# Performance work log

Measured on AMD Instinct MI355X. Metric: run time of the kernel, lower is better.

Reference implementation:

```python
import jax, jax.numpy as jnp
import numpy as np

B, M, L, D = 4, 128, 512, 768
NEG = -1e30


def setup_inputs() -> dict:
    key = jax.random.key(0)
    k1, k2 = jax.random.split(key)
    h = jax.random.normal(k1, (B, L, D), dtype=jnp.float32)
    mention_masks = jax.random.randint(k2, (B, M, L), 0, 2, dtype=jnp.int32)
    return {"h": h, "mention_masks": mention_masks}


def reference(h, mention_masks):
    # h: [B, L, D]; mention_masks: [B, M, L] (0/1)
    # Faithful to: m = (mask == 0).float() * -1e30; (m + h).max(dim=2)
    m = (mention_masks == 0).astype(h.dtype) * NEG          # [B, M, L]
    # broadcast add then max over token dim L -> [B, M, D]
    mention_reprs = jnp.max(h[:, None, :, :] + m[:, :, :, None], axis=2)
    return mention_reprs
```

## Files before the change

### kernel.cpp

```cpp
#include <hip/hip_runtime.h>

#define BB 4
#define MM 128
#define LL 512
#define DD 768
#define NEGF (-1e30f)

__global__ __launch_bounds__(256, 3) void mention_max_part(
    const float* __restrict__ h, const int* __restrict__ mask,
    float* __restrict__ ws)
{
    const int lane = threadIdx.x & 63;
    const int wave = threadIdx.x >> 6;
    const int dch  = blockIdx.x;
    const int mch  = blockIdx.y >> 1;
    const int lh   = blockIdx.y & 1;
    const int b    = blockIdx.z;

    const int d0 = dch * 128 + lane * 2;
    const int m0 = mch * 8;
    const int l0 = lh * 256 + wave * 64;

    const unsigned NEGB = __float_as_uint(NEGF);

    const int* mp = mask + ((size_t)(b * MM + m0)) * LL + l0 + lane;
    unsigned blo[8], bhi[8];
#pragma unroll
    for (int m = 0; m < 8; ++m) {
        unsigned long long bits = __ballot(mp[m * LL] != 0);
        blo[m] = (unsigned)bits;
        bhi[m] = (unsigned)(bits >> 32);
    }

    float2 acc[8];
#pragma unroll
    for (int m = 0; m < 8; ++m) acc[m] = make_float2(NEGF, NEGF);

#pragma unroll
    for (int s = 0; s < 2; ++s) {
        const float2* hp =
            (const float2*)(h + ((size_t)(b * LL + l0 + s * 32)) * DD + d0);
        float2 hreg[32];
#pragma unroll
        for (int i = 0; i < 32; ++i) hreg[i] = hp[(size_t)i * (DD / 2)];

#pragma unroll
        for (int m = 0; m < 8; ++m) {
            const unsigned w32 = s ? bhi[m] : blo[m];
            float ax = acc[m].x, ay = acc[m].y;
#pragma unroll
            for (int i = 0; i < 32; i += 2) {
                const unsigned r0 = (unsigned)((int)(w32 << (31 - i)) >> 31);
                const unsigned r1 = (unsigned)((int)(w32 << (30 - i)) >> 31);
                const float ad0 = __uint_as_float(~r0 & NEGB);
                const float ad1 = __uint_as_float(~r1 & NEGB);
                ax = fmaxf(ax, fmaxf(hreg[i].x + ad0, hreg[i + 1].x + ad1));
                ay = fmaxf(ay, fmaxf(hreg[i].y + ad0, hreg[i + 1].y + ad1));
            }
            acc[m].x = ax;
            acc[m].y = ay;
        }
    }

    __shared__ float2 red[4][8][64];
#pragma unroll
    for (int m = 0; m < 8; ++m) red[wave][m][lane] = acc[m];
    __syncthreads();

#pragma unroll
    for (int r = 0; r < 2; ++r) {
        const int o  = (int)threadIdx.x + r * 256;
        const int m  = o >> 6;
        const int dp = o & 63;
        float2 v = red[0][m][dp];
#pragma unroll
        for (int w = 1; w < 4; ++w) {
            const float2 u = red[w][m][dp];
            v.x = fmaxf(v.x, u.x);
            v.y = fmaxf(v.y, u.y);
        }
        ((float2*)(ws + ((size_t)lh * BB * MM * DD) +
                   ((size_t)(b * MM + m0 + m)) * DD + dch * 128))[dp] = v;
    }
}

__global__ __launch_bounds__(256) void mention_max_merge(
    const float* __restrict__ ws, float* __restrict__ out)
{
    const int i = (int)(blockIdx.x * blockDim.x + threadIdx.x);
    const float4* p0 = (const float4*)ws;
    const float4* p1 = (const float4*)(ws + (size_t)BB * MM * DD);
    const float4 a = p0[i], b = p1[i];
    float4 v;
    v.x = fmaxf(a.x, b.x);
    v.y = fmaxf(a.y, b.y);
    v.z = fmaxf(a.z, b.z);
    v.w = fmaxf(a.w, b.w);
    ((float4*)out)[i] = v;
}

extern "C" void kernel_launch(void* const* d_in, const int* in_sizes, int n_in,
                              void* d_out, int out_size, void* d_ws, size_t ws_size,
                              hipStream_t stream) {
    const float* h    = (const float*)d_in[0];
    const int*   mask = (const int*)d_in[1];
    float*       out  = (float*)d_out;
    float*       ws   = (float*)d_ws;
    dim3 grid1(DD / 128, (MM / 8) * 2, BB);
    mention_max_part<<<grid1, dim3(256), 0, stream>>>(h, mask, ws);
    const int n4 = BB * MM * DD / 4;
    mention_max_merge<<<n4 / 256, dim3(256), 0, stream>>>(ws, out);
}
```

Baseline: 74.18 us.

## Widen per-thread columns to float4 and split tokens into four partial chunks

New measurement: 72.32 us. 1.03x faster.

```diff
diff --git a/kernel.cpp b/kernel.cpp
--- a/kernel.cpp
+++ b/kernel.cpp
@@ -13,56 +13,55 @@
     const int lane = threadIdx.x & 63;
     const int wave = threadIdx.x >> 6;
     const int dch  = blockIdx.x;
-    const int mch  = blockIdx.y >> 1;
-    const int lh   = blockIdx.y & 1;
+    const int mch  = blockIdx.y >> 2;
+    const int lh   = blockIdx.y & 3;
     const int b    = blockIdx.z;
 
-    const int d0 = dch * 128 + lane * 2;
+    const int d0 = dch * 256 + lane * 4;
     const int m0 = mch * 8;
-    const int l0 = lh * 256 + wave * 64;
+    const int l0 = lh * 128 + wave * 32;
 
-    const unsigned NEGB = __float_as_uint(NEGF);
+    const int lclamp = (l0 + lane < LL) ? (l0 + lane) : (LL - 1);
+    const int* mp = mask + ((size_t)(b * MM + m0)) * LL + lclamp;
 
-    const int* mp = mask + ((size_t)(b * MM + m0)) * LL + l0 + lane;
-    unsigned blo[8], bhi[8];
+    unsigned bits[8];
 #pragma unroll
     for (int m = 0; m < 8; ++m) {
-        unsigned long long bits = __ballot(mp[m * LL] != 0);
-        blo[m] = (unsigned)bits;
-        bhi[m] = (unsigned)(bits >> 32);
+        unsigned long long bl = __ballot(mp[m * LL] != 0);
+        bits[m] = (unsigned)__builtin_amdgcn_readfirstlane((int)(unsigned)bl);
     }
 
-    float2 acc[8];
+    float4 acc[8];
 #pragma unroll
-    for (int m = 0; m < 8; ++m) acc[m] = make_float2(NEGF, NEGF);
+    for (int m = 0; m < 8; ++m) acc[m] = make_float4(NEGF, NEGF, NEGF, NEGF);
 
 #pragma unroll
     for (int s = 0; s < 2; ++s) {
-        const float2* hp =
-            (const float2*)(h + ((size_t)(b * LL + l0 + s * 32)) * DD + d0);
-        float2 hreg[32];
+        const float4* hp =
+            (const float4*)(h + ((size_t)(b * LL + l0 + s * 16)) * DD + d0);
+        float4 hreg[16];
 #pragma unroll
-        for (int i = 0; i < 32; ++i) hreg[i] = hp[(size_t)i * (DD / 2)];
+        for (int i = 0; i < 16; ++i) hreg[i] = hp[(size_t)i * (DD / 4)];
 
 #pragma unroll
         for (int m = 0; m < 8; ++m) {
-            const unsigned w32 = s ? bhi[m] : blo[m];
-            float ax = acc[m].x, ay = acc[m].y;
+            const unsigned w = bits[m];
+            float4 a = acc[m];
 #pragma unroll
-            for (int i = 0; i < 32; i += 2) {
-                const unsigned r0 = (unsigned)((int)(w32 << (31 - i)) >> 31);
-                const unsigned r1 = (unsigned)((int)(w32 << (30 - i)) >> 31);
-                const float ad0 = __uint_as_float(~r0 & NEGB);
-                const float ad1 = __uint_as_float(~r1 & NEGB);
-                ax = fmaxf(ax, fmaxf(hreg[i].x + ad0, hreg[i + 1].x + ad1));
-                ay = fmaxf(ay, fmaxf(hreg[i].y + ad0, hreg[i + 1].y + ad1));
+            for (int i = 0; i < 16; i += 2) {
+                const int k = s * 16 + i;
+                const float ad0 = ((w >> k) & 1u) ? 0.0f : NEGF;
+                const float ad1 = ((w >> (k + 1)) & 1u) ? 0.0f : NEGF;
+                a.x = fmaxf(fmaxf(hreg[i].x + ad0, hreg[i + 1].x + ad1), a.x);
+                a.y = fmaxf(fmaxf(hreg[i].y + ad0, hreg[i + 1].y + ad1), a.y);
+                a.z = fmaxf(fmaxf(hreg[i].z + ad0, hreg[i + 1].z + ad1), a.z);
+                a.w = fmaxf(fmaxf(hreg[i].w + ad0, hreg[i + 1].w + ad1), a.w);
             }
-            acc[m].x = ax;
-            acc[m].y = ay;
+            acc[m] = a;
         }
     }
 
-    __shared__ float2 red[4][8][64];
+    __shared__ float4 red[4][8][64];
 #pragma unroll
     for (int m = 0; m < 8; ++m) red[wave][m][lane] = acc[m];
     __syncthreads();
@@ -72,15 +71,17 @@
         const int o  = (int)threadIdx.x + r * 256;
         const int m  = o >> 6;
         const int dp = o & 63;
-        float2 v = red[0][m][dp];
+        float4 v = red[0][m][dp];
 #pragma unroll
         for (int w = 1; w < 4; ++w) {
-            const float2 u = red[w][m][dp];
+            const float4 u = red[w][m][dp];
             v.x = fmaxf(v.x, u.x);
             v.y = fmaxf(v.y, u.y);
+            v.z = fmaxf(v.z, u.z);
+            v.w = fmaxf(v.w, u.w);
         }
-        ((float2*)(ws + ((size_t)lh * BB * MM * DD) +
-                   ((size_t)(b * MM + m0 + m)) * DD + dch * 128))[dp] = v;
+        ((float4*)(ws + ((size_t)lh * BB * MM * DD) +
+                   ((size_t)(b * MM + m0 + m)) * DD + dch * 256))[dp] = v;
     }
 }
 
@@ -88,14 +89,16 @@
     const float* __restrict__ ws, float* __restrict__ out)
 {
     const int i = (int)(blockIdx.x * blockDim.x + threadIdx.x);
-    const float4* p0 = (const float4*)ws;
-    const float4* p1 = (const float4*)(ws + (size_t)BB * MM * DD);
-    const float4 a = p0[i], b = p1[i];
-    float4 v;
-    v.x = fmaxf(a.x, b.x);
-    v.y = fmaxf(a.y, b.y);
-    v.z = fmaxf(a.z, b.z);
-    v.w = fmaxf(a.w, b.w);
+    const size_t half = (size_t)BB * MM * DD;
+    float4 v = ((const float4*)ws)[i];
+#pragma unroll
+    for (int p = 1; p < 4; ++p) {
+        const float4 u = ((const float4*)(ws + p * half))[i];
+        v.x = fmaxf(v.x, u.x);
+        v.y = fmaxf(v.y, u.y);
+        v.z = fmaxf(v.z, u.z);
+        v.w = fmaxf(v.w, u.w);
+    }
     ((float4*)out)[i] = v;
 }
 
@@ -106,7 +109,7 @@
     const int*   mask = (const int*)d_in[1];
     float*       out  = (float*)d_out;
     float*       ws   = (float*)d_ws;
-    dim3 grid1(DD / 128, (MM / 8) * 2, BB);
+    dim3 grid1(DD / 256, (MM / 8) * 4, BB);
     mention_max_part<<<grid1, dim3(256), 0, stream>>>(h, mask, ws);
     const int n4 = BB * MM * DD / 4;
     mention_max_merge<<<n4 / 256, dim3(256), 0, stream>>>(ws, out);
```
